# Performance work log

Hardware: AMD Instinct MI355X
Metric: run time of the kernel (lower is better)

The kernel has to match this reference:

```python
import jax, jax.numpy as jnp
import numpy as np

N_NODES = 100000
N_EDGES = 3200000
NUM_TYPES = 8
TYPE_DIM = 16
IN_DIM = 5
HID = 64
HEADS = 2
OUT = 64
LN_EPS = 1e-5
NEG_SLOPE = 0.2


def segment_softmax(logits, seg, num_segments):
    # logits: [E, H], seg: [E] destination ids
    m = jax.ops.segment_max(logits, seg, num_segments=num_segments)
    m = jnp.where(jnp.isfinite(m), m, 0.0)
    e = jnp.exp(logits - m[seg])
    s = jax.ops.segment_sum(e, seg, num_segments=num_segments)
    return e / (s[seg] + 1e-16)


def gat_conv(x, W, a_src, a_dst, b, src, dst, n_nodes, heads, ch):
    # x: [N, F_in], W: [F_in, heads*ch], a_src/a_dst: [heads, ch], b: [heads*ch]
    h = (x @ W).reshape(n_nodes, heads, ch)            # [N, H, C]
    al_s = jnp.einsum('nhc,hc->nh', h, a_src)          # [N, H]
    al_d = jnp.einsum('nhc,hc->nh', h, a_dst)          # [N, H]
    e = jax.nn.leaky_relu(al_s[src] + al_d[dst], NEG_SLOPE)  # [E, H]
    alpha = segment_softmax(e, dst, n_nodes)           # [E, H]
    msg = alpha[:, :, None] * h[src]                   # [E, H, C]
    out = jax.ops.segment_sum(msg, dst, num_segments=n_nodes)  # [N, H, C]
    return out.reshape(n_nodes, heads * ch) + b


def setup_inputs() -> dict:
    key = jax.random.key(0)
    ks = jax.random.split(key, 16)
    in1 = IN_DIM + TYPE_DIM  # 21
    inp = {
        'x': jax.random.normal(ks[0], (N_NODES, IN_DIM), dtype=jnp.float32),
        'edge_index': jax.random.randint(ks[1], (2, N_EDGES), 0, N_NODES, dtype=jnp.int32),
        'type_ids': jax.random.randint(ks[2], (N_NODES,), 0, NUM_TYPES, dtype=jnp.int32),
        'type_emb': jax.random.normal(ks[3], (NUM_TYPES, TYPE_DIM), dtype=jnp.float32) * 0.3,
        'W1': jax.random.normal(ks[4], (in1, HID), dtype=jnp.float32) * (1.0 / np.sqrt(in1)),
        'a_src1': jax.random.normal(ks[5], (HEADS, HID // HEADS), dtype=jnp.float32) * 0.1,
        'a_dst1': jax.random.normal(ks[6], (HEADS, HID // HEADS), dtype=jnp.float32) * 0.1,
        'b1': jnp.zeros((HID,), dtype=jnp.float32),
        'W2': jax.random.normal(ks[7], (HID, OUT), dtype=jnp.float32) * (1.0 / np.sqrt(HID)),
        'a_src2': jax.random.normal(ks[8], (1, OUT), dtype=jnp.float32) * 0.1,
        'a_dst2': jax.random.normal(ks[9], (1, OUT), dtype=jnp.float32) * 0.1,
        'b2': jnp.zeros((OUT,), dtype=jnp.float32),
        'gamma': jnp.ones((OUT,), dtype=jnp.float32),
        'beta': jnp.zeros((OUT,), dtype=jnp.float32),
    }
    return inp


def reference(x, type_emb, W1, a_src1, a_dst1, b1, W2, a_src2, a_dst2, b2, gamma, beta, edge_index, type_ids):
    n = x.shape[0]
    # type embedding concat
    xin = jnp.concatenate([x, type_emb[type_ids]], axis=1)  # [N, 21]
    # add self loops (PyG GATConv default)
    loops = jnp.arange(n, dtype=edge_index.dtype)
    src = jnp.concatenate([edge_index[0], loops])
    dst = jnp.concatenate([edge_index[1], loops])
    h = gat_conv(xin, W1, a_src1, a_dst1, b1, src, dst, n, HEADS, HID // HEADS)
    h = jax.nn.relu(h)  # dropout = identity at inference
    h = gat_conv(h, W2, a_src2, a_dst2, b2, src, dst, n, 1, OUT)
    # LayerNorm
    mu = jnp.mean(h, axis=-1, keepdims=True)
    var = jnp.var(h, axis=-1, keepdims=True)
    return (h - mu) / jnp.sqrt(var + LN_EPS) * gamma + beta
```

## Files before the change

### kernel.cpp

```cpp
#include <hip/hip_runtime.h>
#include <hip/hip_fp16.h>

#define NEG_SLOPE 0.2f
#define BKT_SHIFT 8
#define BKT_NODES 256
#define BKT_CAP 10240
#define SRC_SHIFT 18
#define SRC_MASK 0x3FFFF
#define CHUNK 4096
#define NBMAX 512

typedef _Float16 half8 __attribute__((ext_vector_type(8)));
typedef float float4v __attribute__((ext_vector_type(4)));

__global__ void k_node1(const float* __restrict__ x, const int* __restrict__ type_ids,
                        const float* __restrict__ type_emb, const float* __restrict__ W1,
                        const float* __restrict__ a_src1, const float* __restrict__ a_dst1,
                        __half2* __restrict__ h1h, float* __restrict__ als1, float* __restrict__ ald1,
                        int N)
{
    int node = blockIdx.x * 4 + (threadIdx.x >> 6);
    int j = threadIdx.x & 63;
    if (node >= N) return;

    float xin[21];
#pragma unroll
    for (int k = 0; k < 5; k++) xin[k] = x[node * 5 + k];
    int t = type_ids[node];
#pragma unroll
    for (int k = 0; k < 16; k++) xin[5 + k] = type_emb[t * 16 + k];

    float h = 0.f;
#pragma unroll
    for (int k = 0; k < 21; k++) h += xin[k] * W1[k * 64 + j];

    float hn = __shfl_xor(h, 1);
    if ((j & 1) == 0)
        h1h[node * 32 + (j >> 1)] = __floats2half2_rn(h, hn);

    int head = j >> 5, lane = j & 31;
    float ps = h * a_src1[head * 32 + lane];
    float pd = h * a_dst1[head * 32 + lane];
#pragma unroll
    for (int m = 16; m >= 1; m >>= 1) { ps += __shfl_xor(ps, m); pd += __shfl_xor(pd, m); }
    if (lane == 0) { als1[node * 2 + head] = ps; ald1[node * 2 + head] = pd; }
}

__global__ void k_bucketA(const int* __restrict__ ei, unsigned int* __restrict__ pk,
                          int* __restrict__ bcnt, int E, int NBKT)
{
    __shared__ unsigned int stage[CHUNK];
    __shared__ unsigned short stageB[CHUNK];
    __shared__ int cnt[NBMAX];
    __shared__ int excl[NBMAX];
    __shared__ int curp[NBMAX];
    __shared__ int gbase[NBMAX];

    int t = threadIdx.x;
    int e0 = blockIdx.x * CHUNK;
    bool vec4 = ((E & 3) == 0);

    for (int i = t; i < NBMAX; i += 256) cnt[i] = 0;
    __syncthreads();

    int4 s4[4], d4[4];
    bool val[4];

    if (vec4) {
#pragma unroll
        for (int it = 0; it < 4; it++) {
            int e = e0 + it * 1024 + t * 4;
            val[it] = (e < E);
            if (val[it]) {
                s4[it] = *(const int4*)(ei + e);
                d4[it] = *(const int4*)(ei + (size_t)E + e);
                atomicAdd(&cnt[d4[it].x >> BKT_SHIFT], 1);
                atomicAdd(&cnt[d4[it].y >> BKT_SHIFT], 1);
                atomicAdd(&cnt[d4[it].z >> BKT_SHIFT], 1);
                atomicAdd(&cnt[d4[it].w >> BKT_SHIFT], 1);
            }
        }
    } else {
        for (int i = t; i < CHUNK; i += 256) {
            int e = e0 + i;
            if (e >= E) break;
            atomicAdd(&cnt[ei[E + e] >> BKT_SHIFT], 1);
        }
    }
    __syncthreads();
    for (int i = t; i < NBMAX; i += 256) curp[i] = cnt[i];
    __syncthreads();
    for (int off = 1; off < NBMAX; off <<= 1) {
        int v0 = (t >= off) ? cnt[t - off] : 0;
        int v1 = (t + 256 >= off) ? cnt[t + 256 - off] : 0;
        __syncthreads();
        cnt[t] += v0; cnt[t + 256] += v1;
        __syncthreads();
    }
    for (int i = t; i < NBMAX; i += 256) {
        int o = curp[i];
        int ex = cnt[i] - o;
        excl[i] = ex;
        curp[i] = ex;
    }
    __syncthreads();
    for (int b = t; b < NBKT; b += 256) {
        int c = cnt[b] - excl[b];
        gbase[b] = (c > 0) ? atomicAdd(&bcnt[b], c) : 0;
    }
    __syncthreads();
    if (vec4) {
#pragma unroll
        for (int it = 0; it < 4; it++) {
            if (!val[it]) continue;
            int ss[4] = {s4[it].x, s4[it].y, s4[it].z, s4[it].w};
            int dd[4] = {d4[it].x, d4[it].y, d4[it].z, d4[it].w};
#pragma unroll
            for (int k = 0; k < 4; k++) {
                int b = dd[k] >> BKT_SHIFT;
                int p = atomicAdd(&curp[b], 1);
                stage[p] = (unsigned)ss[k] | ((unsigned)(dd[k] & (BKT_NODES - 1)) << SRC_SHIFT);
                stageB[p] = (unsigned short)b;
            }
        }
    } else {
        for (int i = t; i < CHUNK; i += 256) {
            int e = e0 + i;
            if (e >= E) break;
            int s = ei[e], d = ei[E + e];
            int b = d >> BKT_SHIFT;
            int p = atomicAdd(&curp[b], 1);
            stage[p] = (unsigned)s | ((unsigned)(d & (BKT_NODES - 1)) << SRC_SHIFT);
            stageB[p] = (unsigned short)b;
        }
    }
    __syncthreads();
    int total = E - e0; if (total > CHUNK) total = CHUNK;
    for (int i = t; i < total; i += 256) {
        int b = stageB[i];
        int idx = gbase[b] + (i - excl[b]);
        if (idx < BKT_CAP) pk[(size_t)b * BKT_CAP + idx] = stage[i];
    }
}

__global__ void k_build(const unsigned int* __restrict__ pk, const int* __restrict__ bcnt,
                        int* __restrict__ rs, int* __restrict__ cur,
                        int* __restrict__ ssrc, int N)
{
    __shared__ unsigned int vals[BKT_CAP];
    __shared__ int cnt[BKT_NODES];
    __shared__ int cursor[BKT_NODES];
    __shared__ int orig[BKT_NODES];
    __shared__ int red[256];
    int b = blockIdx.x;
    int t = threadIdx.x;
    int nb = min(bcnt[b], BKT_CAP);

    int part = 0;
    for (int i = t; i < b; i += 256) part += min(bcnt[i], BKT_CAP);
    red[t] = part;
    cnt[t] = 0;
    __syncthreads();
    for (int off = 128; off; off >>= 1) {
        if (t < off) red[t] += red[t + off];
        __syncthreads();
    }
    int bs = red[0];

    const unsigned int* mypk = pk + (size_t)b * BKT_CAP;
    int nb4 = nb & ~3;
    for (int e = t * 4; e < nb4; e += 1024) {
        uint4 v = *(const uint4*)(mypk + e);
        *(uint4*)(vals + e) = v;
        atomicAdd(&cnt[v.x >> SRC_SHIFT], 1);
        atomicAdd(&cnt[v.y >> SRC_SHIFT], 1);
        atomicAdd(&cnt[v.z >> SRC_SHIFT], 1);
        atomicAdd(&cnt[v.w >> SRC_SHIFT], 1);
    }
    for (int e = nb4 + t; e < nb; e += 256) {
        unsigned int v = mypk[e];
        vals[e] = v;
        atomicAdd(&cnt[v >> SRC_SHIFT], 1);
    }
    __syncthreads();
    orig[t] = cnt[t];
    __syncthreads();
    for (int off = 1; off < BKT_NODES; off <<= 1) {
        int v = (t >= off) ? cnt[t - off] : 0;
        __syncthreads();
        cnt[t] += v;
        __syncthreads();
    }
    {
        int c = orig[t];
        int ex = cnt[t] - c;
        cursor[t] = ex;
        int node = (b << BKT_SHIFT) + t;
        if (node < N) { rs[node] = bs + ex; cur[node] = bs + ex + c; }
    }
    __syncthreads();
    for (int e = t; e < nb; e += 256) {
        unsigned int w = vals[e];
        int p = atomicAdd(&cursor[w >> SRC_SHIFT], 1);
        ssrc[bs + p] = (int)(w & SRC_MASK);
    }
}

__global__ void k_gather1(const int* __restrict__ rs, const int* __restrict__ cur,
                          const int* __restrict__ ssrc, const float4* __restrict__ h4,
                          const float* __restrict__ als1, const float* __restrict__ ald1,
                          const float* __restrict__ b1, float4* __restrict__ h2h4, int N)
{
    int node = blockIdx.x * 4 + (threadIdx.x >> 6);
    if (node >= N) return;
    int l = threadIdx.x & 63;
    int eg = l >> 3;
    int ch = l & 7;
    int head = ch >> 2;
    float ad = ald1[node * 2 + head];

    int beg = rs[node], end = cur[node];
    int cnt = end - beg;
    __half2 acc2[4];
    acc2[0] = acc2[1] = acc2[2] = acc2[3] = __float2half2_rn(0.f);
    float wsum = 0.f;

    int s0n = (eg < cnt) ? ssrc[beg + eg] : node;
    int s1n = (8 + eg < cnt) ? ssrc[beg + 8 + eg] : node;

    for (int base = 0; base < cnt; base += 16) {
        int s0 = s0n, s1 = s1n;
        bool v0 = (base + eg) < cnt, v1 = (base + 8 + eg) < cnt;
        int n0 = base + 16 + eg, n1 = base + 24 + eg;
        s0n = (n0 < cnt) ? ssrc[beg + n0] : node;
        s1n = (n1 < cnt) ? ssrc[beg + n1] : node;

        float al0 = als1[s0 * 2 + head];
        float al1 = als1[s1 * 2 + head];
        float4 r0 = h4[(size_t)s0 * 8 + ch];
        float4 r1 = h4[(size_t)s1 * 8 + ch];
        float lg0 = al0 + ad; lg0 = (lg0 >= 0.f) ? lg0 : NEG_SLOPE * lg0;
        float lg1 = al1 + ad; lg1 = (lg1 >= 0.f) ? lg1 : NEG_SLOPE * lg1;
        float w0 = v0 ? __expf(lg0) : 0.f;
        float w1 = v1 ? __expf(lg1) : 0.f;
        __half2 wh0 = __float2half2_rn(w0);
        __half2 wh1 = __float2half2_rn(w1);
        const __half2* p0 = (const __half2*)&r0;
        const __half2* p1 = (const __half2*)&r1;
#pragma unroll
        for (int q = 0; q < 4; q++) {
            acc2[q] = __hfma2(p0[q], wh0, acc2[q]);
            acc2[q] = __hfma2(p1[q], wh1, acc2[q]);
        }
        wsum += w0 + w1;
    }
    float acc[8];
#pragma unroll
    for (int q = 0; q < 4; q++) {
        float2 f = __half22float2(acc2[q]);
        acc[2*q] = f.x; acc[2*q+1] = f.y;
    }
#pragma unroll
    for (int m = 8; m <= 32; m <<= 1) {
        wsum += __shfl_xor(wsum, m);
#pragma unroll
        for (int q = 0; q < 8; q++) acc[q] += __shfl_xor(acc[q], m);
    }
    {
        float lg = als1[node * 2 + head] + ad;
        lg = (lg >= 0.f) ? lg : NEG_SLOPE * lg;
        float w = __expf(lg);
        float4 r = h4[(size_t)node * 8 + ch];
        const __half2* p = (const __half2*)&r;
#pragma unroll
        for (int q = 0; q < 4; q++) {
            float2 f = __half22float2(p[q]);
            acc[2*q] += w * f.x; acc[2*q+1] += w * f.y;
        }
        wsum += w;
    }
    float inv = 1.f / (wsum + 1e-16f);
    if (eg == 0) {
        union { float4 f4; __half2 h2[4]; } u;
#pragma unroll
        for (int q = 0; q < 4; q++) {
            float v0 = fmaxf(acc[2*q]   * inv + b1[ch * 8 + 2*q],     0.f);
            float v1 = fmaxf(acc[2*q+1] * inv + b1[ch * 8 + 2*q + 1], 0.f);
            u.h2[q] = __floats2half2_rn(v0, v1);
        }
        h2h4[(size_t)node * 8 + ch] = u.f4;
    }
}

__global__ __launch_bounds__(256) void k_node2m(
        const _Float16* __restrict__ h2h, const float* __restrict__ W2,
        const float* __restrict__ a_src2, const float* __restrict__ a_dst2,
        _Float16* __restrict__ h3h, float* __restrict__ als2, float* __restrict__ ald2, int N)
{
    __shared__ _Float16 w2t[64][72];
    __shared__ float h3t[4][16][65];
    int t = threadIdx.x;
    for (int e = t; e < 4096; e += 256) {
        int k = e >> 6, n = e & 63;
        w2t[n][k] = (_Float16)W2[e];
    }
    __syncthreads();

    int w = t >> 6, l = t & 63;
    int l15 = l & 15, quad = l >> 4;
    int nodebase = blockIdx.x * 64 + w * 16;

    int arow = nodebase + l15;
    if (arow >= N) arow = N - 1;
    const half8* ap = (const half8*)(h2h + (size_t)arow * 64 + quad * 8);
    half8 a0 = ap[0];
    half8 a1 = ap[4];
    float4v accs[4];
#pragma unroll
    for (int nt = 0; nt < 4; nt++) {
        half8 b0 = *(const half8*)(&w2t[nt * 16 + l15][quad * 8]);
        half8 b1 = *(const half8*)(&w2t[nt * 16 + l15][32 + quad * 8]);
        float4v c = {0.f, 0.f, 0.f, 0.f};
        c = __builtin_amdgcn_mfma_f32_16x16x32_f16(a0, b0, c, 0, 0, 0);
        c = __builtin_amdgcn_mfma_f32_16x16x32_f16(a1, b1, c, 0, 0, 0);
        accs[nt] = c;
    }
#pragma unroll
    for (int nt = 0; nt < 4; nt++)
#pragma unroll
        for (int r = 0; r < 4; r++)
            h3t[w][quad * 4 + r][nt * 16 + l15] = accs[nt][r];
    __syncthreads();

    int m = l >> 2, part = l & 3;
    int g = blockIdx.x * 64 + w * 16 + m;
    float ps = 0.f, pd = 0.f;
    union { float4 f4[2]; _Float16 h[16]; } u;
#pragma unroll
    for (int c = 0; c < 16; c++) {
        float v = h3t[w][m][part * 16 + c];
        ps += v * a_src2[part * 16 + c];
        pd += v * a_dst2[part * 16 + c];
        u.h[c] = (_Float16)v;
    }
    if (g < N) {
        float4* dst = (float4*)(h3h + (size_t)g * 64) + part * 2;
        dst[0] = u.f4[0];
        dst[1] = u.f4[1];
    }
    ps += __shfl_xor(ps, 1); ps += __shfl_xor(ps, 2);
    pd += __shfl_xor(pd, 1); pd += __shfl_xor(pd, 2);
    if (part == 0 && g < N) { als2[g] = ps; ald2[g] = pd; }
}

__global__ void k_gather2(const int* __restrict__ rs, const int* __restrict__ cur,
                          const int* __restrict__ ssrc, const float4* __restrict__ h4,
                          const float* __restrict__ als2, const float* __restrict__ ald2,
                          const float* __restrict__ b2, const float* __restrict__ gamma,
                          const float* __restrict__ beta, float* __restrict__ out, int N)
{
    int node = blockIdx.x * 4 + (threadIdx.x >> 6);
    if (node >= N) return;
    int l = threadIdx.x & 63;
    int eg = l >> 3;
    int ch = l & 7;
    float ad = ald2[node];

    int beg = rs[node], end = cur[node];
    int cnt = end - beg;
    __half2 acc2[4];
    acc2[0] = acc2[1] = acc2[2] = acc2[3] = __float2half2_rn(0.f);
    float wsum = 0.f;

    int s0n = (eg < cnt) ? ssrc[beg + eg] : node;
    int s1n = (8 + eg < cnt) ? ssrc[beg + 8 + eg] : node;

    for (int base = 0; base < cnt; base += 16) {
        int s0 = s0n, s1 = s1n;
        bool v0 = (base + eg) < cnt, v1 = (base + 8 + eg) < cnt;
        int n0 = base + 16 + eg, n1 = base + 24 + eg;
        s0n = (n0 < cnt) ? ssrc[beg + n0] : node;
        s1n = (n1 < cnt) ? ssrc[beg + n1] : node;

        float al0 = als2[s0];
        float al1 = als2[s1];
        float4 r0 = h4[(size_t)s0 * 8 + ch];
        float4 r1 = h4[(size_t)s1 * 8 + ch];
        float lg0 = al0 + ad; lg0 = (lg0 >= 0.f) ? lg0 : NEG_SLOPE * lg0;
        float lg1 = al1 + ad; lg1 = (lg1 >= 0.f) ? lg1 : NEG_SLOPE * lg1;
        float w0 = v0 ? __expf(lg0) : 0.f;
        float w1 = v1 ? __expf(lg1) : 0.f;
        __half2 wh0 = __float2half2_rn(w0);
        __half2 wh1 = __float2half2_rn(w1);
        const __half2* p0 = (const __half2*)&r0;
        const __half2* p1 = (const __half2*)&r1;
#pragma unroll
        for (int q = 0; q < 4; q++) {
            acc2[q] = __hfma2(p0[q], wh0, acc2[q]);
            acc2[q] = __hfma2(p1[q], wh1, acc2[q]);
        }
        wsum += w0 + w1;
    }
    float acc[8];
#pragma unroll
    for (int q = 0; q < 4; q++) {
        float2 f = __half22float2(acc2[q]);
        acc[2*q] = f.x; acc[2*q+1] = f.y;
    }
#pragma unroll
    for (int m = 8; m <= 32; m <<= 1) {
        wsum += __shfl_xor(wsum, m);
#pragma unroll
        for (int q = 0; q < 8; q++) acc[q] += __shfl_xor(acc[q], m);
    }
    {
        float lg = als2[node] + ad;
        lg = (lg >= 0.f) ? lg : NEG_SLOPE * lg;
        float w = __expf(lg);
        float4 r = h4[(size_t)node * 8 + ch];
        const __half2* p = (const __half2*)&r;
#pragma unroll
        for (int q = 0; q < 4; q++) {
            float2 f = __half22float2(p[q]);
            acc[2*q] += w * f.x; acc[2*q+1] += w * f.y;
        }
        wsum += w;
    }
    float inv = 1.f / (wsum + 1e-16f);
    float o[8];
    float s = 0.f;
#pragma unroll
    for (int q = 0; q < 8; q++) { o[q] = acc[q] * inv + b2[ch * 8 + q]; s += o[q]; }
#pragma unroll
    for (int m = 1; m <= 4; m <<= 1) s += __shfl_xor(s, m);
    float mu = s * (1.f / 64.f);
    float v = 0.f;
#pragma unroll
    for (int q = 0; q < 8; q++) { float d = o[q] - mu; v += d * d; }
#pragma unroll
    for (int m = 1; m <= 4; m <<= 1) v += __shfl_xor(v, m);
    v *= (1.f / 64.f);
    float r = rsqrtf(v + 1e-5f);
    if (eg == 0) {
        float res[8];
#pragma unroll
        for (int q = 0; q < 8; q++)
            res[q] = (o[q] - mu) * r * gamma[ch * 8 + q] + beta[ch * 8 + q];
        float4* op = (float4*)(out + (size_t)node * 64 + ch * 8);
        op[0] = make_float4(res[0], res[1], res[2], res[3]);
        op[1] = make_float4(res[4], res[5], res[6], res[7]);
    }
}

extern "C" void kernel_launch(void* const* d_in, const int* in_sizes, int n_in,
                              void* d_out, int out_size, void* d_ws, size_t ws_size,
                              hipStream_t stream) {
    const float* x        = (const float*)d_in[0];
    const int*   ei       = (const int*)  d_in[1];
    const int*   type_ids = (const int*)  d_in[2];
    const float* type_emb = (const float*)d_in[3];
    const float* W1       = (const float*)d_in[4];
    const float* a_src1   = (const float*)d_in[5];
    const float* a_dst1   = (const float*)d_in[6];
    const float* b1       = (const float*)d_in[7];
    const float* W2       = (const float*)d_in[8];
    const float* a_src2   = (const float*)d_in[9];
    const float* a_dst2   = (const float*)d_in[10];
    const float* b2       = (const float*)d_in[11];
    const float* gamma    = (const float*)d_in[12];
    const float* beta     = (const float*)d_in[13];

    int N = in_sizes[0] / 5;
    int E = in_sizes[1] / 2;
    int NBKT = (N + BKT_NODES - 1) >> BKT_SHIFT;

    char* base = (char*)d_ws;
    size_t off = 0;
    auto carve = [&](size_t bytes) { void* p = base + off; off += (bytes + 255) & ~(size_t)255; return p; };
    __half2* h1h = (__half2*)carve((size_t)N * 64 * sizeof(__half));
    size_t pk_bytes = (size_t)NBKT * BKT_CAP * sizeof(unsigned int);
    size_t h23_bytes = 2 * (size_t)N * 64 * sizeof(__half);
    char* uni = (char*)carve(pk_bytes > h23_bytes ? pk_bytes : h23_bytes);
    _Float16* h2h = (_Float16*)uni;
    _Float16* h3h = (_Float16*)(uni + (size_t)N * 64 * sizeof(__half));
    unsigned int* pk = (unsigned int*)uni;
    float* als1  = (float*)carve((size_t)N * 2 * sizeof(float));
    float* ald1  = (float*)carve((size_t)N * 2 * sizeof(float));
    float* als2  = (float*)carve((size_t)N * sizeof(float));
    float* ald2  = (float*)carve((size_t)N * sizeof(float));
    int*   rs    = (int*)carve((size_t)N * sizeof(int));
    int*   cur   = (int*)carve((size_t)N * sizeof(int));
    int*   bcnt  = (int*)carve(1024 * sizeof(int));
    int*   ssrc  = (int*)carve((size_t)E * sizeof(int));

    dim3 tb(256);
    dim3 nb((N + 3) / 4);

    k_node1<<<nb, tb, 0, stream>>>(x, type_ids, type_emb, W1, a_src1, a_dst1,
                                   h1h, als1, ald1, N);

    hipMemsetAsync(bcnt, 0, NBKT * sizeof(int), stream);
    k_bucketA<<<dim3((E + CHUNK - 1) / CHUNK), tb, 0, stream>>>(ei, pk, bcnt, E, NBKT);
    k_build<<<dim3(NBKT), tb, 0, stream>>>(pk, bcnt, rs, cur, ssrc, N);

    k_gather1<<<nb, tb, 0, stream>>>(rs, cur, ssrc, (const float4*)h1h, als1, ald1, b1,
                                     (float4*)h2h, N);
    k_node2m<<<dim3((N + 63) / 64), tb, 0, stream>>>(h2h, W2, a_src2, a_dst2,
                                                     h3h, als2, ald2, N);
    k_gather2<<<nb, tb, 0, stream>>>(rs, cur, ssrc, (const float4*)h3h, als2, ald2, b2,
                                     gamma, beta, (float*)d_out, N);
}
```

Before: 317.1 us.

## Map one node per 8-lane group in gather kernels, broadcasting sources via shuffles

Both gather kernels now assign 8 lanes per destination node (8 nodes per wavefront) instead of one full wavefront per node. Each lane loads one source index and attention weight per step, and the group broadcasts them with shuffles so every lane fetches its 16-byte channel slice. This drops the cross-lane reduction of partial accumulators and accumulates in fp32 instead of half2. In exchange, groups in a wavefront iterate to the maximum degree among their 8 nodes, which adds divergence, and the loads per step are serialized over 8 sources.

```diff
diff --git a/kernel.cpp b/kernel.cpp
--- a/kernel.cpp
+++ b/kernel.cpp
@@ -211,84 +211,84 @@
                           const float* __restrict__ als1, const float* __restrict__ ald1,
                           const float* __restrict__ b1, float4* __restrict__ h2h4, int N)
 {
-    int node = blockIdx.x * 4 + (threadIdx.x >> 6);
-    if (node >= N) return;
-    int l = threadIdx.x & 63;
-    int eg = l >> 3;
-    int ch = l & 7;
-    int head = ch >> 2;
-    float ad = ald1[node * 2 + head];
-
-    int beg = rs[node], end = cur[node];
-    int cnt = end - beg;
-    __half2 acc2[4];
-    acc2[0] = acc2[1] = acc2[2] = acc2[3] = __float2half2_rn(0.f);
+    int t = threadIdx.x;
+    int wv = t >> 6, l = t & 63;
+    int g = l >> 3, i = l & 7;
+    int head = i >> 2;
+    int grpbase = l & 56;
+
+    int node = blockIdx.x * 32 + wv * 8 + g;
+    bool live = node < N;
+    int node_c = live ? node : (N - 1);
+
+    int beg = rs[node_c];
+    int cnt = live ? (cur[node_c] - beg) : 0;
+
+    float ad0 = ald1[node_c * 2 + 0];
+    float ad1 = ald1[node_c * 2 + 1];
+    float ad = head ? ad1 : ad0;
+
+    int mc = cnt;
+    mc = max(mc, __shfl_xor(mc, 8));
+    mc = max(mc, __shfl_xor(mc, 16));
+    mc = max(mc, __shfl_xor(mc, 32));
+
+    float acc[8];
+#pragma unroll
+    for (int k = 0; k < 8; k++) acc[k] = 0.f;
     float wsum = 0.f;
 
-    int s0n = (eg < cnt) ? ssrc[beg + eg] : node;
-    int s1n = (8 + eg < cnt) ? ssrc[beg + 8 + eg] : node;
-
-    for (int base = 0; base < cnt; base += 16) {
-        int s0 = s0n, s1 = s1n;
-        bool v0 = (base + eg) < cnt, v1 = (base + 8 + eg) < cnt;
-        int n0 = base + 16 + eg, n1 = base + 24 + eg;
-        s0n = (n0 < cnt) ? ssrc[beg + n0] : node;
-        s1n = (n1 < cnt) ? ssrc[beg + n1] : node;
-
-        float al0 = als1[s0 * 2 + head];
-        float al1 = als1[s1 * 2 + head];
-        float4 r0 = h4[(size_t)s0 * 8 + ch];
-        float4 r1 = h4[(size_t)s1 * 8 + ch];
-        float lg0 = al0 + ad; lg0 = (lg0 >= 0.f) ? lg0 : NEG_SLOPE * lg0;
-        float lg1 = al1 + ad; lg1 = (lg1 >= 0.f) ? lg1 : NEG_SLOPE * lg1;
-        float w0 = v0 ? __expf(lg0) : 0.f;
-        float w1 = v1 ? __expf(lg1) : 0.f;
-        __half2 wh0 = __float2half2_rn(w0);
-        __half2 wh1 = __float2half2_rn(w1);
-        const __half2* p0 = (const __half2*)&r0;
-        const __half2* p1 = (const __half2*)&r1;
-#pragma unroll
-        for (int q = 0; q < 4; q++) {
-            acc2[q] = __hfma2(p0[q], wh0, acc2[q]);
-            acc2[q] = __hfma2(p1[q], wh1, acc2[q]);
-        }
-        wsum += w0 + w1;
-    }
-    float acc[8];
-#pragma unroll
-    for (int q = 0; q < 4; q++) {
-        float2 f = __half22float2(acc2[q]);
-        acc[2*q] = f.x; acc[2*q+1] = f.y;
-    }
-#pragma unroll
-    for (int m = 8; m <= 32; m <<= 1) {
-        wsum += __shfl_xor(wsum, m);
-#pragma unroll
-        for (int q = 0; q < 8; q++) acc[q] += __shfl_xor(acc[q], m);
-    }
+    for (int b = 0; b < mc; b += 8) {
+        int slot = b + i;
+        bool valid = slot < cnt;
+        int idx = valid ? (beg + slot) : 0;
+        int s = ssrc[idx];
+        if (!valid) s = node_c;
+        float2 al = *(const float2*)(als1 + (size_t)s * 2);
+        float lg0 = al.x + ad0; lg0 = (lg0 >= 0.f) ? lg0 : NEG_SLOPE * lg0;
+        float lg1 = al.y + ad1; lg1 = (lg1 >= 0.f) ? lg1 : NEG_SLOPE * lg1;
+        float w0 = valid ? __expf(lg0) : 0.f;
+        float w1 = valid ? __expf(lg1) : 0.f;
+        __half2 wp = __floats2half2_rn(w0, w1);
+        unsigned wpi = *(unsigned*)&wp;
+
+#pragma unroll
+        for (int r = 0; r < 8; r++) {
+            int sr = __shfl(s, grpbase + r);
+            unsigned wri = __shfl(wpi, grpbase + r);
+            __half2 wh = *(__half2*)&wri;
+            float w = head ? __high2float(wh) : __low2float(wh);
+            float4 rv = h4[(size_t)sr * 8 + i];
+            const __half* hp = (const __half*)&rv;
+#pragma unroll
+            for (int k = 0; k < 8; k++)
+                acc[k] = fmaf(w, __half2float(hp[k]), acc[k]);
+            wsum += w;
+        }
+    }
+
     {
-        float lg = als1[node * 2 + head] + ad;
+        float lg = als1[node_c * 2 + head] + ad;
         lg = (lg >= 0.f) ? lg : NEG_SLOPE * lg;
         float w = __expf(lg);
-        float4 r = h4[(size_t)node * 8 + ch];
-        const __half2* p = (const __half2*)&r;
+        float4 rv = h4[(size_t)node_c * 8 + i];
+        const __half* hp = (const __half*)&rv;
+#pragma unroll
+        for (int k = 0; k < 8; k++)
+            acc[k] = fmaf(w, __half2float(hp[k]), acc[k]);
+        wsum += w;
+    }
+
+    float inv = 1.f / (wsum + 1e-16f);
+    if (live) {
+        union { float4 f4; __half2 h2[4]; } u;
 #pragma unroll
         for (int q = 0; q < 4; q++) {
-            float2 f = __half22float2(p[q]);
-            acc[2*q] += w * f.x; acc[2*q+1] += w * f.y;
-        }
-        wsum += w;
-    }
-    float inv = 1.f / (wsum + 1e-16f);
-    if (eg == 0) {
-        union { float4 f4; __half2 h2[4]; } u;
-#pragma unroll
-        for (int q = 0; q < 4; q++) {
-            float v0 = fmaxf(acc[2*q]   * inv + b1[ch * 8 + 2*q],     0.f);
-            float v1 = fmaxf(acc[2*q+1] * inv + b1[ch * 8 + 2*q + 1], 0.f);
+            float v0 = fmaxf(acc[2*q]   * inv + b1[i * 8 + 2*q],     0.f);
+            float v1 = fmaxf(acc[2*q+1] * inv + b1[i * 8 + 2*q + 1], 0.f);
             u.h2[q] = __floats2half2_rn(v0, v1);
         }
-        h2h4[(size_t)node * 8 + ch] = u.f4;
+        h2h4[(size_t)node * 8 + i] = u.f4;
     }
 }
 
@@ -359,94 +359,83 @@
                           const float* __restrict__ b2, const float* __restrict__ gamma,
                           const float* __restrict__ beta, float* __restrict__ out, int N)
 {
-    int node = blockIdx.x * 4 + (threadIdx.x >> 6);
-    if (node >= N) return;
-    int l = threadIdx.x & 63;
-    int eg = l >> 3;
-    int ch = l & 7;
-    float ad = ald2[node];
-
-    int beg = rs[node], end = cur[node];
-    int cnt = end - beg;
-    __half2 acc2[4];
-    acc2[0] = acc2[1] = acc2[2] = acc2[3] = __float2half2_rn(0.f);
+    int t = threadIdx.x;
+    int wv = t >> 6, l = t & 63;
+    int g = l >> 3, i = l & 7;
+    int grpbase = l & 56;
+
+    int node = blockIdx.x * 32 + wv * 8 + g;
+    bool live = node < N;
+    int node_c = live ? node : (N - 1);
+
+    int beg = rs[node_c];
+    int cnt = live ? (cur[node_c] - beg) : 0;
+    float ad = ald2[node_c];
+
+    int mc = cnt;
+    mc = max(mc, __shfl_xor(mc, 8));
+    mc = max(mc, __shfl_xor(mc, 16));
+    mc = max(mc, __shfl_xor(mc, 32));
+
+    float acc[8];
+#pragma unroll
+    for (int k = 0; k < 8; k++) acc[k] = 0.f;
     float wsum = 0.f;
 
-    int s0n = (eg < cnt) ? ssrc[beg + eg] : node;
-    int s1n = (8 + eg < cnt) ? ssrc[beg + 8 + eg] : node;
-
-    for (int base = 0; base < cnt; base += 16) {
-        int s0 = s0n, s1 = s1n;
-        bool v0 = (base + eg) < cnt, v1 = (base + 8 + eg) < cnt;
-        int n0 = base + 16 + eg, n1 = base + 24 + eg;
-        s0n = (n0 < cnt) ? ssrc[beg + n0] : node;
-        s1n = (n1 < cnt) ? ssrc[beg + n1] : node;
-
-        float al0 = als2[s0];
-        float al1 = als2[s1];
-        float4 r0 = h4[(size_t)s0 * 8 + ch];
-        float4 r1 = h4[(size_t)s1 * 8 + ch];
-        float lg0 = al0 + ad; lg0 = (lg0 >= 0.f) ? lg0 : NEG_SLOPE * lg0;
-        float lg1 = al1 + ad; lg1 = (lg1 >= 0.f) ? lg1 : NEG_SLOPE * lg1;
-        float w0 = v0 ? __expf(lg0) : 0.f;
-        float w1 = v1 ? __expf(lg1) : 0.f;
-        __half2 wh0 = __float2half2_rn(w0);
-        __half2 wh1 = __float2half2_rn(w1);
-        const __half2* p0 = (const __half2*)&r0;
-        const __half2* p1 = (const __half2*)&r1;
-#pragma unroll
-        for (int q = 0; q < 4; q++) {
-            acc2[q] = __hfma2(p0[q], wh0, acc2[q]);
-            acc2[q] = __hfma2(p1[q], wh1, acc2[q]);
-        }
-        wsum += w0 + w1;
-    }
-    float acc[8];
-#pragma unroll
-    for (int q = 0; q < 4; q++) {
-        float2 f = __half22float2(acc2[q]);
-        acc[2*q] = f.x; acc[2*q+1] = f.y;
-    }
-#pragma unroll
-    for (int m = 8; m <= 32; m <<= 1) {
-        wsum += __shfl_xor(wsum, m);
-#pragma unroll
-        for (int q = 0; q < 8; q++) acc[q] += __shfl_xor(acc[q], m);
-    }
+    for (int b = 0; b < mc; b += 8) {
+        int slot = b + i;
+        bool valid = slot < cnt;
+        int idx = valid ? (beg + slot) : 0;
+        int s = ssrc[idx];
+        if (!valid) s = node_c;
+        float lg = als2[s] + ad;
+        lg = (lg >= 0.f) ? lg : NEG_SLOPE * lg;
+        float w = valid ? __expf(lg) : 0.f;
+
+#pragma unroll
+        for (int r = 0; r < 8; r++) {
+            int sr = __shfl(s, grpbase + r);
+            float wr = __shfl(w, grpbase + r);
+            float4 rv = h4[(size_t)sr * 8 + i];
+            const __half* hp = (const __half*)&rv;
+#pragma unroll
+            for (int k = 0; k < 8; k++)
+                acc[k] = fmaf(wr, __half2float(hp[k]), acc[k]);
+            wsum += wr;
+        }
+    }
+
     {
-        float lg = als2[node] + ad;
+        float lg = als2[node_c] + ad;
         lg = (lg >= 0.f) ? lg : NEG_SLOPE * lg;
         float w = __expf(lg);
-        float4 r = h4[(size_t)node * 8 + ch];
-        const __half2* p = (const __half2*)&r;
-#pragma unroll
-        for (int q = 0; q < 4; q++) {
-            float2 f = __half22float2(p[q]);
-            acc[2*q] += w * f.x; acc[2*q+1] += w * f.y;
-        }
+        float4 rv = h4[(size_t)node_c * 8 + i];
+        const __half* hp = (const __half*)&rv;
+#pragma unroll
+        for (int k = 0; k < 8; k++)
+            acc[k] = fmaf(w, __half2float(hp[k]), acc[k]);
         wsum += w;
     }
+
     float inv = 1.f / (wsum + 1e-16f);
     float o[8];
     float s = 0.f;
 #pragma unroll
-    for (int q = 0; q < 8; q++) { o[q] = acc[q] * inv + b2[ch * 8 + q]; s += o[q]; }
-#pragma unroll
-    for (int m = 1; m <= 4; m <<= 1) s += __shfl_xor(s, m);
+    for (int k = 0; k < 8; k++) { o[k] = acc[k] * inv + b2[i * 8 + k]; s += o[k]; }
+    s += __shfl_xor(s, 1); s += __shfl_xor(s, 2); s += __shfl_xor(s, 4);
     float mu = s * (1.f / 64.f);
     float v = 0.f;
 #pragma unroll
-    for (int q = 0; q < 8; q++) { float d = o[q] - mu; v += d * d; }
-#pragma unroll
-    for (int m = 1; m <= 4; m <<= 1) v += __shfl_xor(v, m);
+    for (int k = 0; k < 8; k++) { float d = o[k] - mu; v += d * d; }
+    v += __shfl_xor(v, 1); v += __shfl_xor(v, 2); v += __shfl_xor(v, 4);
     v *= (1.f / 64.f);
-    float r = rsqrtf(v + 1e-5f);
-    if (eg == 0) {
+    float rstd = rsqrtf(v + 1e-5f);
+    if (live) {
         float res[8];
 #pragma unroll
-        for (int q = 0; q < 8; q++)
-            res[q] = (o[q] - mu) * r * gamma[ch * 8 + q] + beta[ch * 8 + q];
-        float4* op = (float4*)(out + (size_t)node * 64 + ch * 8);
+        for (int k = 0; k < 8; k++)
+            res[k] = (o[k] - mu) * rstd * gamma[i * 8 + k] + beta[i * 8 + k];
+        float4* op = (float4*)(out + (size_t)node * 64 + i * 8);
         op[0] = make_float4(res[0], res[1], res[2], res[3]);
         op[1] = make_float4(res[4], res[5], res[6], res[7]);
     }
@@ -491,22 +480,22 @@
     int*   rs    = (int*)carve((size_t)N * sizeof(int));
     int*   cur   = (int*)carve((size_t)N * sizeof(int));
     int*   bcnt  = (int*)carve(1024 * sizeof(int));
-    int*   ssrc  = (int*)carve((size_t)E * sizeof(int));
+    int*   ssrc  = (int*)carve((size_t)E * sizeof(int) + 256);
 
     dim3 tb(256);
-    dim3 nb((N + 3) / 4);
-
-    k_node1<<<nb, tb, 0, stream>>>(x, type_ids, type_emb, W1, a_src1, a_dst1,
-                                   h1h, als1, ald1, N);
+
+    k_node1<<<dim3((N + 3) / 4), tb, 0, stream>>>(x, type_ids, type_emb, W1, a_src1, a_dst1,
+                                                  h1h, als1, ald1, N);
 
     hipMemsetAsync(bcnt, 0, NBKT * sizeof(int), stream);
     k_bucketA<<<dim3((E + CHUNK - 1) / CHUNK), tb, 0, stream>>>(ei, pk, bcnt, E, NBKT);
     k_build<<<dim3(NBKT), tb, 0, stream>>>(pk, bcnt, rs, cur, ssrc, N);
 
-    k_gather1<<<nb, tb, 0, stream>>>(rs, cur, ssrc, (const float4*)h1h, als1, ald1, b1,
+    dim3 ng((N + 31) / 32);
+    k_gather1<<<ng, tb, 0, stream>>>(rs, cur, ssrc, (const float4*)h1h, als1, ald1, b1,
                                      (float4*)h2h, N);
     k_node2m<<<dim3((N + 63) / 64), tb, 0, stream>>>(h2h, W2, a_src2, a_dst2,
                                                      h3h, als2, ald2, N);
-    k_gather2<<<nb, tb, 0, stream>>>(rs, cur, ssrc, (const float4*)h3h, als2, ald2, b2,
+    k_gather2<<<ng, tb, 0, stream>>>(rs, cur, ssrc, (const float4*)h3h, als2, ald2, b2,
                                      gamma, beta, (float*)d_out, N);
 }
```

New measurement: 324.2 us. 1.02x slower.
